# Performance work log

Measured on AMD Instinct MI355X. Metric: run time of the kernel, lower is better.

Reference implementation:

```python
import jax, jax.numpy as jnp
import numpy as np

EMBED_DIM = 1024
NUM_HEADS = 16
HEAD_DIM = EMBED_DIM // NUM_HEADS  # 64


def setup_inputs() -> dict:
    key = jax.random.key(0)
    ks = jax.random.split(key, 9)
    B, S, E, D = 4, 2048, EMBED_DIM, HEAD_DIM
    s_e = 1.0 / np.sqrt(E)
    return {
        "x": jax.random.normal(ks[0], (B, S, E), dtype=jnp.float32),
        "Wq": jax.random.uniform(ks[1], (E, E), jnp.float32, -s_e, s_e),
        "bq": jax.random.uniform(ks[2], (E,), jnp.float32, -s_e, s_e),
        "Wk": jax.random.uniform(ks[3], (E, D), jnp.float32, -s_e, s_e),
        "bk": jax.random.uniform(ks[4], (D,), jnp.float32, -s_e, s_e),
        "Wv": jax.random.uniform(ks[5], (E, D), jnp.float32, -s_e, s_e),
        "bv": jax.random.uniform(ks[6], (D,), jnp.float32, -s_e, s_e),
        "Wo": jax.random.uniform(ks[7], (E, E), jnp.float32, -s_e, s_e),
        "bo": jax.random.uniform(ks[8], (E,), jnp.float32, -s_e, s_e),
    }


def reference(x, Wq, bq, Wk, bk, Wv, bv, Wo, bo):
    B, S, E = x.shape
    H, D = NUM_HEADS, HEAD_DIM
    q = (x @ Wq + bq).reshape(B, S, H, D)           # [B,S,H,D]
    k = x @ Wk + bk                                  # [B,S,D] shared single K head
    v = x @ Wv + bv                                  # [B,S,D] shared single V head
    scale = 1.0 / jnp.sqrt(jnp.asarray(D, x.dtype))
    # broadcast shared K across query heads: [B,H,Sq,Sk]
    scores = jnp.einsum("bqhd,bkd->bhqk", q, k) * scale
    probs = jax.nn.softmax(scores, axis=-1)
    out = jnp.einsum("bhqk,bkd->bqhd", probs, v).reshape(B, S, E)
    return out @ Wo + bo
```

## Files before the change

kernel.cpp:

```cpp
#include <hip/hip_runtime.h>

typedef short  bf16x8 __attribute__((ext_vector_type(8)));
typedef float  f32x4  __attribute__((ext_vector_type(4)));
typedef float  f32x16 __attribute__((ext_vector_type(16)));
typedef unsigned int u32;

__device__ __forceinline__ ushort f2b(float f) {
    union { float f; unsigned u; } c; c.f = f;
    unsigned r = c.u + 0x7fffu + ((c.u >> 16) & 1u);
    return (ushort)(r >> 16);
}

__device__ __forceinline__ unsigned cvtpk(float lo, float hi) {
    unsigned r;
    asm("v_cvt_pk_bf16_f32 %0, %1, %2" : "=v"(r) : "v"(lo), "v"(hi));
    return r;
}

__device__ __forceinline__ float fexp2(float x) {
#if __has_builtin(__builtin_amdgcn_exp2f)
    return __builtin_amdgcn_exp2f(x);
#else
    float r; asm("v_exp_f32 %0, %1" : "=v"(r) : "v"(x)); return r;
#endif
}

__device__ __forceinline__ void gload_lds16(const void* g, void* l) {
    __builtin_amdgcn_global_load_lds(
        (const __attribute__((address_space(1))) u32*)g,
        (__attribute__((address_space(3))) u32*)l, 16, 0, 0);
}

__global__ __launch_bounds__(256) void cast_f32_bf16(const float* __restrict__ in,
                                                     ushort* __restrict__ out, int n) {
    for (int i = (blockIdx.x * blockDim.x + threadIdx.x) * 4; i < n;
         i += gridDim.x * blockDim.x * 4) {
        float4 v = *(const float4*)(in + i);
        ushort4 o;
        o.x = f2b(v.x); o.y = f2b(v.y); o.z = f2b(v.z); o.w = f2b(v.w);
        *(ushort4*)(out + i) = o;
    }
}

__global__ __launch_bounds__(256) void transpose_cast2(const float* __restrict__ in0,
                                                       ushort* __restrict__ out0,
                                                       const float* __restrict__ in1,
                                                       ushort* __restrict__ out1,
                                                       int R, int C) {
    __shared__ float tile[32][33];
    const float* in = blockIdx.z ? in1 : in0;
    ushort* out = blockIdx.z ? out1 : out0;
    int c0 = blockIdx.x * 32, r0 = blockIdx.y * 32;
    int tx = threadIdx.x, ty = threadIdx.y;
#pragma unroll
    for (int i = 0; i < 32; i += 8)
        tile[ty + i][tx] = in[(size_t)(r0 + ty + i) * C + c0 + tx];
    __syncthreads();
#pragma unroll
    for (int i = 0; i < 32; i += 8)
        out[(size_t)(c0 + ty + i) * R + r0 + tx] = f2b(tile[tx][ty + i]);
}

__global__ void concat_bias3(const float* __restrict__ bq, const float* __restrict__ bk,
                             const float* __restrict__ bv, float* __restrict__ o) {
    for (int i = threadIdx.x; i < 1152; i += 256)
        o[i] = (i < 1024) ? bq[i] : (i < 1088) ? bk[i - 1024] : bv[i - 1088];
}

__global__ __launch_bounds__(256) void repack_kv(const ushort* __restrict__ qkv,
                                                 ushort* __restrict__ Kc,
                                                 ushort* __restrict__ Vc) {
    __shared__ ushort vl[64][72];
    int t = blockIdx.x, b = blockIdx.y;
    int tid = threadIdx.x;
#pragma unroll
    for (int u = tid; u < 512; u += 256) {
        int s = u >> 3, c = u & 7;
        const ushort* src = qkv + (size_t)(b * 2048 + t * 64 + s) * 1152 + 1024 + c * 8;
        *(uint4*)(Kc + ((size_t)(b * 8 + c) * 2048 + t * 64 + s) * 8) = *(const uint4*)src;
        *(uint4*)(&vl[s][c * 8]) = *(const uint4*)(src + 64);
    }
    __syncthreads();
#pragma unroll
    for (int u = tid; u < 512; u += 256) {
        int sc = u >> 6, d = u & 63;
        ushort tmp[8];
#pragma unroll
        for (int si = 0; si < 8; si++) tmp[si] = vl[sc * 8 + si][d];
        *(uint4*)(Vc + ((size_t)((b * 32 + t) * 8 + sc) * 64 + d) * 8) = *(uint4*)tmp;
    }
}

template <bool OUT_BF16>
__global__ __launch_bounds__(256) void gemm_bt(const ushort* __restrict__ A,
                                               const ushort* __restrict__ BT,
                                               const float* __restrict__ bias,
                                               void* __restrict__ Y, int M, int N, int K,
                                               int nq, float scale) {
    __shared__ ushort As[128 * 64];
    __shared__ ushort Bs[128 * 64];

    int nwg = gridDim.x * gridDim.y;
    int bid = blockIdx.y * gridDim.x + blockIdx.x;
    int swz = (bid & 7) * (nwg >> 3) + (bid >> 3);
    int bx = swz % gridDim.x, by = swz / gridDim.x;

    int m0 = by * 128, n0 = bx * 128;
    int t = threadIdx.x;
    int lane = t & 63, wid = t >> 6;
    int wr = wid >> 1, wc = wid & 1;
    int fr = lane & 15, fg = lane >> 4;

    int srow = wid * 32 + (lane >> 3);
    int scol = (lane & 7) * 8;
    const ushort* asrc = A + (size_t)(m0 + srow) * K + scol;
    const ushort* bsrc = BT + (size_t)(n0 + srow) * K + scol;

    f32x4 acc[4][4] = {};

    for (int kb = 0; kb < K; kb += 64) {
#pragma unroll
        for (int op = 0; op < 4; op++) {
            gload_lds16(asrc + kb + (size_t)op * 8 * K, &As[(wid * 32 + op * 8) * 64]);
            gload_lds16(bsrc + kb + (size_t)op * 8 * K, &Bs[(wid * 32 + op * 8) * 64]);
        }
        __syncthreads();
#pragma unroll
        for (int kk = 0; kk < 2; kk++) {
            bf16x8 af[4], bfr[4];
#pragma unroll
            for (int m = 0; m < 4; m++)
                af[m] = *(const bf16x8*)&As[(wr * 64 + m * 16 + fr) * 64 + kk * 32 + fg * 8];
#pragma unroll
            for (int n = 0; n < 4; n++)
                bfr[n] = *(const bf16x8*)&Bs[(wc * 64 + n * 16 + fr) * 64 + kk * 32 + fg * 8];
#pragma unroll
            for (int m = 0; m < 4; m++)
#pragma unroll
                for (int n = 0; n < 4; n++)
                    acc[m][n] = __builtin_amdgcn_mfma_f32_16x16x32_bf16(
                        af[m], bfr[n], acc[m][n], 0, 0, 0);
        }
        __syncthreads();
    }

#pragma unroll
    for (int m = 0; m < 4; m++)
#pragma unroll
        for (int n = 0; n < 4; n++) {
            int col = n0 + wc * 64 + n * 16 + fr;
            float bv = bias[col];
            float sc = (col < nq) ? scale : 1.0f;
#pragma unroll
            for (int j = 0; j < 4; j++) {
                int row = m0 + wr * 64 + m * 16 + fg * 4 + j;
                float v = (acc[m][n][j] + bv) * sc;
                if (OUT_BF16)
                    ((ushort*)Y)[(size_t)row * N + col] = f2b(v);
                else
                    ((float*)Y)[(size_t)row * N + col] = v;
            }
        }
}

__global__ __launch_bounds__(256, 4) void attn_kernel(const ushort* __restrict__ qkv,
                                                      const ushort* __restrict__ Kc,
                                                      const ushort* __restrict__ Vc,
                                                      ushort* __restrict__ ctx) {
    const int S = 2048, E = 1024, QSTR = 1152;
    __shared__ ushort Kb[2][4096];
    __shared__ ushort Vb[2][4096];

    int b = blockIdx.z, h = blockIdx.y;
    int wid = threadIdx.x >> 6, lane = threadIdx.x & 63;
    int q0 = blockIdx.x * 128 + wid * 32;
    int ql = lane & 31, hi = lane >> 5;

    int c0 = wid * 2, c1 = c0 + 1;
    const ushort* ks0 = Kc + (size_t)(b * 8 + c0) * 2048 * 8 + lane * 8;
    const ushort* ks1 = Kc + (size_t)(b * 8 + c1) * 2048 * 8 + lane * 8;
    const ushort* vs0 = Vc + (size_t)(b * 32 * 8 + c0) * 64 * 8 + lane * 8;
    const ushort* vs1 = Vc + (size_t)(b * 32 * 8 + c1) * 64 * 8 + lane * 8;

    const ushort* qbase = qkv + (size_t)(b * S + q0 + ql) * QSTR + h * 64 + hi * 8;
    bf16x8 qf0 = *(const bf16x8*)(qbase);
    bf16x8 qf1 = *(const bf16x8*)(qbase + 16);
    bf16x8 qf2 = *(const bf16x8*)(qbase + 32);
    bf16x8 qf3 = *(const bf16x8*)(qbase + 48);

    const ushort* kb0 = &Kb[0][hi * 512 + ql * 8];
    const ushort* vb0 = &Vb[0][hi * 512 + ql * 8];

    f32x16 acc0 = {}, acc1 = {};
    f32x16 lv = {};

    gload_lds16(ks0, &Kb[0][c0 * 512]);
    gload_lds16(ks1, &Kb[0][c1 * 512]);
    gload_lds16(vs0, &Vb[0][c0 * 512]);
    gload_lds16(vs1, &Vb[0][c1 * 512]);
    __syncthreads();

    int cur = 0;
    for (int t = 0; t < 32; ++t) {
        if (t < 31) {
            int nb = cur ^ 1;
            ks0 += 512; ks1 += 512; vs0 += 4096; vs1 += 4096;
            gload_lds16(ks0, &Kb[nb][c0 * 512]);
            gload_lds16(ks1, &Kb[nb][c1 * 512]);
            gload_lds16(vs0, &Vb[nb][c0 * 512]);
            gload_lds16(vs1, &Vb[nb][c1 * 512]);
        }
        const ushort* kp = kb0 + cur * 4096;
        const ushort* vp = vb0 + cur * 4096;

        f32x16 pt0 = {}, pt1 = {};
        __builtin_amdgcn_s_setprio(1);
#pragma unroll
        for (int s = 0; s < 4; s++) {
            bf16x8 kf0 = *(const bf16x8*)(kp + s * 1024);
            bf16x8 kf1 = *(const bf16x8*)(kp + s * 1024 + 256);
            bf16x8 qs = (s == 0) ? qf0 : (s == 1) ? qf1 : (s == 2) ? qf2 : qf3;
            pt0 = __builtin_amdgcn_mfma_f32_32x32x16_bf16(kf0, qs, pt0, 0, 0, 0);
            pt1 = __builtin_amdgcn_mfma_f32_32x32x16_bf16(kf1, qs, pt1, 0, 0, 0);
        }
        __builtin_amdgcn_s_setprio(0);

#pragma unroll
        for (int r = 0; r < 16; r++) pt0[r] = fexp2(pt0[r]);
#pragma unroll
        for (int r = 0; r < 16; r++) pt1[r] = fexp2(pt1[r]);

        __builtin_amdgcn_s_setprio(1);
#pragma unroll
        for (int ks = 0; ks < 4; ks++) {
            float p0, p1, p2, p3, p4, p5, p6, p7;
            if (ks == 0)      { p0=pt0[0]; p1=pt0[1]; p2=pt0[2]; p3=pt0[3];
                                p4=pt0[4]; p5=pt0[5]; p6=pt0[6]; p7=pt0[7]; }
            else if (ks == 1) { p0=pt0[8]; p1=pt0[9]; p2=pt0[10]; p3=pt0[11];
                                p4=pt0[12]; p5=pt0[13]; p6=pt0[14]; p7=pt0[15]; }
            else if (ks == 2) { p0=pt1[0]; p1=pt1[1]; p2=pt1[2]; p3=pt1[3];
                                p4=pt1[4]; p5=pt1[5]; p6=pt1[6]; p7=pt1[7]; }
            else              { p0=pt1[8]; p1=pt1[9]; p2=pt1[10]; p3=pt1[11];
                                p4=pt1[12]; p5=pt1[13]; p6=pt1[14]; p7=pt1[15]; }
            unsigned w0 = cvtpk(p0, p1);
            unsigned w2 = cvtpk(p4, p5);
            asm volatile("v_permlane32_swap_b32 %0, %1" : "+v"(w0), "+v"(w2));
            unsigned w1 = cvtpk(p2, p3);
            unsigned w3 = cvtpk(p6, p7);
            asm volatile("v_permlane32_swap_b32 %0, %1" : "+v"(w1), "+v"(w3));
            bf16x8 pa;
            ((unsigned*)&pa)[0] = w0;
            ((unsigned*)&pa)[1] = w1;
            ((unsigned*)&pa)[2] = w2;
            ((unsigned*)&pa)[3] = w3;

            bf16x8 va0 = *(const bf16x8*)(vp + ks * 1024);
            bf16x8 va1 = *(const bf16x8*)(vp + ks * 1024 + 256);
            acc0 = __builtin_amdgcn_mfma_f32_32x32x16_bf16(va0, pa, acc0, 0, 0, 0);
            acc1 = __builtin_amdgcn_mfma_f32_32x32x16_bf16(va1, pa, acc1, 0, 0, 0);
        }
        __builtin_amdgcn_s_setprio(0);

        lv = lv + pt0;
        lv = lv + pt1;

        __syncthreads();
        cur ^= 1;
    }

    float v[16];
#pragma unroll
    for (int r = 0; r < 16; r++) v[r] = lv[r];
#pragma unroll
    for (int st = 8; st; st >>= 1)
#pragma unroll
        for (int r = 0; r < 8; r++)
            if (r < st) v[r] = v[r] + v[r + st];
    float l = v[0] + __shfl_xor(v[0], 32);
    float inv = 1.f / l;

    ushort* obase = ctx + (size_t)(b * S + q0 + ql) * E + h * 64;
#pragma unroll
    for (int g = 0; g < 4; g++) {
        int d = 8 * g + 4 * hi;
        ushort4 o;
        o.x = f2b(acc0[4 * g + 0] * inv);
        o.y = f2b(acc0[4 * g + 1] * inv);
        o.z = f2b(acc0[4 * g + 2] * inv);
        o.w = f2b(acc0[4 * g + 3] * inv);
        *(ushort4*)(obase + d) = o;
    }
#pragma unroll
    for (int g = 0; g < 4; g++) {
        int d = 32 + 8 * g + 4 * hi;
        ushort4 o;
        o.x = f2b(acc1[4 * g + 0] * inv);
        o.y = f2b(acc1[4 * g + 1] * inv);
        o.z = f2b(acc1[4 * g + 2] * inv);
        o.w = f2b(acc1[4 * g + 3] * inv);
        *(ushort4*)(obase + d) = o;
    }
}

extern "C" void kernel_launch(void* const* d_in, const int* in_sizes, int n_in,
                              void* d_out, int out_size, void* d_ws, size_t ws_size,
                              hipStream_t stream) {
    const int B = 4, S = 2048, E = 1024, D = 64;
    const int M = B * S;
    const int NQKV = 1152;
    const float QSCALE = 0.18033688011112042f;

    const float* x  = (const float*)d_in[0];
    const float* Wq = (const float*)d_in[1];
    const float* bq = (const float*)d_in[2];
    const float* Wk = (const float*)d_in[3];
    const float* bk = (const float*)d_in[4];
    const float* Wv = (const float*)d_in[5];
    const float* bv = (const float*)d_in[6];
    const float* Wo = (const float*)d_in[7];
    const float* bo = (const float*)d_in[8];
    float* out = (float*)d_out;

    char* w = (char*)d_ws;
    ushort* xb    = (ushort*)w;                w += (size_t)M * E * 2;
    ushort* qkv   = (ushort*)w;                w += (size_t)M * NQKV * 2;
    ushort* ctx   = (ushort*)w;                w += (size_t)M * E * 2;
    ushort* WqkvT = (ushort*)w;                w += (size_t)NQKV * E * 2;
    ushort* WoT   = (ushort*)w;                w += (size_t)E * E * 2;
    ushort* Kc    = (ushort*)w;                w += (size_t)B * 8 * S * 8 * 2;
    ushort* Vc    = (ushort*)w;                w += (size_t)B * 32 * 8 * 64 * 8 * 2;
    float*  bqkv  = (float*)w;                 w += 8192;

    cast_f32_bf16<<<2048, 256, 0, stream>>>(x, xb, M * E);
    transpose_cast2<<<dim3(32, 32, 2), dim3(32, 8), 0, stream>>>(
        Wq, WqkvT, Wo, WoT, E, E);
    transpose_cast2<<<dim3(2, 32, 2), dim3(32, 8), 0, stream>>>(
        Wk, WqkvT + (size_t)1024 * E, Wv, WqkvT + (size_t)1088 * E, E, D);
    concat_bias3<<<1, 256, 0, stream>>>(bq, bk, bv, bqkv);

    gemm_bt<true><<<dim3(NQKV / 128, M / 128), 256, 0, stream>>>(
        xb, WqkvT, bqkv, qkv, M, NQKV, E, 1024, QSCALE);
    repack_kv<<<dim3(32, 4), 256, 0, stream>>>(qkv, Kc, Vc);

    attn_kernel<<<dim3(S / 128, 16, B), 256, 0, stream>>>(qkv, Kc, Vc, ctx);

    gemm_bt<false><<<dim3(E / 128, M / 128), 256, 0, stream>>>(
        ctx, WoT, bo, (void*)out, M, E, E, 0, 1.0f);
}
```

Before: 174.6 us.

## Fuse weight prep kernels, write K/V repack from GEMM epilogue, MFMA row-sum

Merges the two transpose-cast launches and the bias concat into one prep_weights kernel. The QKV GEMM epilogue now writes K and V straight into the attention-friendly Kc/Vc layouts, which removes the separate repack_kv kernel. In attention, the softmax denominator is accumulated by an extra MFMA against a ones vector in place of a vector add plus a reduction tree, and the s_setprio hints are removed. In exchange, the scattered 2-byte epilogue stores to Kc/Vc are uncoalesced, and the additional MFMA per step adds matrix-core work.

```diff
diff --git a/kernel.cpp b/kernel.cpp
--- a/kernel.cpp
+++ b/kernel.cpp
@@ -42,16 +42,40 @@
     }
 }
 
-__global__ __launch_bounds__(256) void transpose_cast2(const float* __restrict__ in0,
-                                                       ushort* __restrict__ out0,
-                                                       const float* __restrict__ in1,
-                                                       ushort* __restrict__ out1,
-                                                       int R, int C) {
+__global__ __launch_bounds__(256) void prep_weights(const float* __restrict__ Wq,
+                                                    const float* __restrict__ Wo,
+                                                    const float* __restrict__ Wk,
+                                                    const float* __restrict__ Wv,
+                                                    const float* __restrict__ bq,
+                                                    const float* __restrict__ bk,
+                                                    const float* __restrict__ bv,
+                                                    ushort* __restrict__ WqkvT,
+                                                    ushort* __restrict__ WoT,
+                                                    float* __restrict__ bqkv) {
     __shared__ float tile[32][33];
-    const float* in = blockIdx.z ? in1 : in0;
-    ushort* out = blockIdx.z ? out1 : out0;
-    int c0 = blockIdx.x * 32, r0 = blockIdx.y * 32;
     int tx = threadIdx.x, ty = threadIdx.y;
+    int z = blockIdx.z;
+    const float* in;
+    ushort* out;
+    int c0, r0 = blockIdx.y * 32;
+    const int R = 1024;
+    if (z == 0)      { in = Wq; out = WqkvT; c0 = blockIdx.x * 32; }
+    else if (z == 1) { in = Wo; out = WoT;   c0 = blockIdx.x * 32; }
+    else {
+        int x = blockIdx.x;
+        if (x == 4) {
+            if (blockIdx.y == 0) {
+                int i0 = ty * 32 + tx;
+                for (int k = i0; k < 1152; k += 256)
+                    bqkv[k] = (k < 1024) ? bq[k] : (k < 1088) ? bk[k - 1024] : bv[k - 1088];
+            }
+            return;
+        }
+        if (x > 4) return;
+        if (x < 2) { in = Wk; out = WqkvT + (size_t)1024 * R; c0 = x * 32; }
+        else       { in = Wv; out = WqkvT + (size_t)1088 * R; c0 = (x - 2) * 32; }
+    }
+    int C = (z == 2) ? 64 : 1024;
 #pragma unroll
     for (int i = 0; i < 32; i += 8)
         tile[ty + i][tx] = in[(size_t)(r0 + ty + i) * C + c0 + tx];
@@ -61,42 +85,14 @@
         out[(size_t)(c0 + ty + i) * R + r0 + tx] = f2b(tile[tx][ty + i]);
 }
 
-__global__ void concat_bias3(const float* __restrict__ bq, const float* __restrict__ bk,
-                             const float* __restrict__ bv, float* __restrict__ o) {
-    for (int i = threadIdx.x; i < 1152; i += 256)
-        o[i] = (i < 1024) ? bq[i] : (i < 1088) ? bk[i - 1024] : bv[i - 1088];
-}
-
-__global__ __launch_bounds__(256) void repack_kv(const ushort* __restrict__ qkv,
-                                                 ushort* __restrict__ Kc,
-                                                 ushort* __restrict__ Vc) {
-    __shared__ ushort vl[64][72];
-    int t = blockIdx.x, b = blockIdx.y;
-    int tid = threadIdx.x;
-#pragma unroll
-    for (int u = tid; u < 512; u += 256) {
-        int s = u >> 3, c = u & 7;
-        const ushort* src = qkv + (size_t)(b * 2048 + t * 64 + s) * 1152 + 1024 + c * 8;
-        *(uint4*)(Kc + ((size_t)(b * 8 + c) * 2048 + t * 64 + s) * 8) = *(const uint4*)src;
-        *(uint4*)(&vl[s][c * 8]) = *(const uint4*)(src + 64);
-    }
-    __syncthreads();
-#pragma unroll
-    for (int u = tid; u < 512; u += 256) {
-        int sc = u >> 6, d = u & 63;
-        ushort tmp[8];
-#pragma unroll
-        for (int si = 0; si < 8; si++) tmp[si] = vl[sc * 8 + si][d];
-        *(uint4*)(Vc + ((size_t)((b * 32 + t) * 8 + sc) * 64 + d) * 8) = *(uint4*)tmp;
-    }
-}
-
-template <bool OUT_BF16>
+template <bool OUT_BF16, bool FUSE_KV>
 __global__ __launch_bounds__(256) void gemm_bt(const ushort* __restrict__ A,
                                                const ushort* __restrict__ BT,
                                                const float* __restrict__ bias,
                                                void* __restrict__ Y, int M, int N, int K,
-                                               int nq, float scale) {
+                                               int nq, float scale,
+                                               ushort* __restrict__ Kc,
+                                               ushort* __restrict__ Vc) {
     __shared__ ushort As[128 * 64];
     __shared__ ushort Bs[128 * 64];
 
@@ -151,14 +147,32 @@
             int col = n0 + wc * 64 + n * 16 + fr;
             float bv = bias[col];
             float sc = (col < nq) ? scale : 1.0f;
-#pragma unroll
-            for (int j = 0; j < 4; j++) {
-                int row = m0 + wr * 64 + m * 16 + fg * 4 + j;
-                float v = (acc[m][n][j] + bv) * sc;
-                if (OUT_BF16)
-                    ((ushort*)Y)[(size_t)row * N + col] = f2b(v);
-                else
-                    ((float*)Y)[(size_t)row * N + col] = v;
+            if (FUSE_KV && col >= nq) {
+                int dd = col - nq;
+                bool isV = dd >= 64;
+                dd &= 63;
+#pragma unroll
+                for (int j = 0; j < 4; j++) {
+                    int row = m0 + wr * 64 + m * 16 + fg * 4 + j;
+                    int bb = row >> 11, s = row & 2047;
+                    ushort hv = f2b(acc[m][n][j] + bv);
+                    if (!isV)
+                        Kc[((size_t)(bb * 8 + (dd >> 3)) * 2048 + s) * 8 + (dd & 7)] = hv;
+                    else {
+                        int tt = s >> 6, scn = (s >> 3) & 7, si = s & 7;
+                        Vc[(((size_t)(bb * 32 + tt) * 8 + scn) * 64 + dd) * 8 + si] = hv;
+                    }
+                }
+            } else {
+#pragma unroll
+                for (int j = 0; j < 4; j++) {
+                    int row = m0 + wr * 64 + m * 16 + fg * 4 + j;
+                    float v = (acc[m][n][j] + bv) * sc;
+                    if (OUT_BF16)
+                        ((ushort*)Y)[(size_t)row * N + col] = f2b(v);
+                    else
+                        ((float*)Y)[(size_t)row * N + col] = v;
+                }
             }
         }
 }
@@ -191,8 +205,10 @@
     const ushort* kb0 = &Kb[0][hi * 512 + ql * 8];
     const ushort* vb0 = &Vb[0][hi * 512 + ql * 8];
 
+    const bf16x8 ones = {0x3F80, 0x3F80, 0x3F80, 0x3F80, 0x3F80, 0x3F80, 0x3F80, 0x3F80};
+
     f32x16 acc0 = {}, acc1 = {};
-    f32x16 lv = {};
+    f32x16 accL = {};
 
     gload_lds16(ks0, &Kb[0][c0 * 512]);
     gload_lds16(ks1, &Kb[0][c1 * 512]);
@@ -214,7 +230,6 @@
         const ushort* vp = vb0 + cur * 4096;
 
         f32x16 pt0 = {}, pt1 = {};
-        __builtin_amdgcn_s_setprio(1);
 #pragma unroll
         for (int s = 0; s < 4; s++) {
             bf16x8 kf0 = *(const bf16x8*)(kp + s * 1024);
@@ -223,14 +238,12 @@
             pt0 = __builtin_amdgcn_mfma_f32_32x32x16_bf16(kf0, qs, pt0, 0, 0, 0);
             pt1 = __builtin_amdgcn_mfma_f32_32x32x16_bf16(kf1, qs, pt1, 0, 0, 0);
         }
-        __builtin_amdgcn_s_setprio(0);
 
 #pragma unroll
         for (int r = 0; r < 16; r++) pt0[r] = fexp2(pt0[r]);
 #pragma unroll
         for (int r = 0; r < 16; r++) pt1[r] = fexp2(pt1[r]);
 
-        __builtin_amdgcn_s_setprio(1);
 #pragma unroll
         for (int ks = 0; ks < 4; ks++) {
             float p0, p1, p2, p3, p4, p5, p6, p7;
@@ -258,26 +271,14 @@
             bf16x8 va1 = *(const bf16x8*)(vp + ks * 1024 + 256);
             acc0 = __builtin_amdgcn_mfma_f32_32x32x16_bf16(va0, pa, acc0, 0, 0, 0);
             acc1 = __builtin_amdgcn_mfma_f32_32x32x16_bf16(va1, pa, acc1, 0, 0, 0);
-        }
-        __builtin_amdgcn_s_setprio(0);
-
-        lv = lv + pt0;
-        lv = lv + pt1;
+            accL = __builtin_amdgcn_mfma_f32_32x32x16_bf16(ones, pa, accL, 0, 0, 0);
+        }
 
         __syncthreads();
         cur ^= 1;
     }
 
-    float v[16];
-#pragma unroll
-    for (int r = 0; r < 16; r++) v[r] = lv[r];
-#pragma unroll
-    for (int st = 8; st; st >>= 1)
-#pragma unroll
-        for (int r = 0; r < 8; r++)
-            if (r < st) v[r] = v[r] + v[r + st];
-    float l = v[0] + __shfl_xor(v[0], 32);
-    float inv = 1.f / l;
+    float inv = 1.f / accL[0];
 
     ushort* obase = ctx + (size_t)(b * S + q0 + ql) * E + h * 64;
 #pragma unroll
@@ -332,18 +333,14 @@
     float*  bqkv  = (float*)w;                 w += 8192;
 
     cast_f32_bf16<<<2048, 256, 0, stream>>>(x, xb, M * E);
-    transpose_cast2<<<dim3(32, 32, 2), dim3(32, 8), 0, stream>>>(
-        Wq, WqkvT, Wo, WoT, E, E);
-    transpose_cast2<<<dim3(2, 32, 2), dim3(32, 8), 0, stream>>>(
-        Wk, WqkvT + (size_t)1024 * E, Wv, WqkvT + (size_t)1088 * E, E, D);
-    concat_bias3<<<1, 256, 0, stream>>>(bq, bk, bv, bqkv);
-
-    gemm_bt<true><<<dim3(NQKV / 128, M / 128), 256, 0, stream>>>(
-        xb, WqkvT, bqkv, qkv, M, NQKV, E, 1024, QSCALE);
-    repack_kv<<<dim3(32, 4), 256, 0, stream>>>(qkv, Kc, Vc);
+    prep_weights<<<dim3(32, 32, 3), dim3(32, 8), 0, stream>>>(
+        Wq, Wo, Wk, Wv, bq, bk, bv, WqkvT, WoT, bqkv);
+
+    gemm_bt<true, true><<<dim3(NQKV / 128, M / 128), 256, 0, stream>>>(
+        xb, WqkvT, bqkv, qkv, M, NQKV, E, 1024, QSCALE, Kc, Vc);
 
     attn_kernel<<<dim3(S / 128, 16, B), 256, 0, stream>>>(qkv, Kc, Vc, ctx);
 
-    gemm_bt<false><<<dim3(E / 128, M / 128), 256, 0, stream>>>(
-        ctx, WoT, bo, (void*)out, M, E, E, 0, 1.0f);
-}
+    gemm_bt<false, false><<<dim3(E / 128, M / 128), 256, 0, stream>>>(
+        ctx, WoT, bo, (void*)out, M, E, E, 0, 1.0f, nullptr, nullptr);
+}
```

New measurement: 173.3 us. No clear change (-0.7%).
